# Kernel tuning notes

Measured on AMD Instinct MI355X. Metric: run time of the kernel, lower is better.

Reference implementation:

```python
import jax, jax.numpy as jnp
import numpy as np

N_NODES = 50000
IN_C, HID, N_CLS = 128, 128, 16
N_EDGES = 800000


def gcn_conv(x, W, b, src, dst, deg_inv_sqrt, n_nodes):
    # PyG GCNConv: h = x @ W; out[dst] += norm * h[src]; out += b
    h = x @ W                                   # [N, out_c]
    norm = deg_inv_sqrt[src] * deg_inv_sqrt[dst]  # [E]
    msgs = h[src] * norm[:, None]               # gather + scale, [E, out_c]
    out = jax.ops.segment_sum(msgs, dst, num_segments=n_nodes)
    return out + b


def setup_inputs() -> dict:
    key = jax.random.key(0)
    k1, k2, k3, k4, k5 = jax.random.split(key, 5)
    x = jax.random.normal(k1, (N_NODES, IN_C), dtype=jnp.float32)
    edge_index = jax.random.randint(k2, (2, N_EDGES), 0, N_NODES, dtype=jnp.int64)
    # glorot-ish params (torch.manual_seed(1234) in source only affects init values)
    def lin(k, fan_in, fan_out):
        s = 1.0 / np.sqrt(fan_in)
        kw, kb = jax.random.split(k)
        W = jax.random.uniform(kw, (fan_in, fan_out), minval=-s, maxval=s, dtype=jnp.float32)
        b = jax.random.uniform(kb, (fan_out,), minval=-s, maxval=s, dtype=jnp.float32)
        return W, b
    W1, b1 = lin(k3, IN_C, HID)
    W2, b2 = lin(k4, HID, HID)
    Wh, bh = lin(k5, HID, N_CLS)
    return {"x": x, "edge_index": edge_index, "W1": W1, "b1": b1,
            "W2": W2, "b2": b2, "Wh": Wh, "bh": bh}


def reference(x, edge_index, W1, b1, W2, b2, Wh, bh):
    n = x.shape[0]
    # add self-loops (PyG GCNConv default add_self_loops=True)
    loops = jnp.arange(n, dtype=edge_index.dtype)
    src = jnp.concatenate([edge_index[0], loops])
    dst = jnp.concatenate([edge_index[1], loops])
    # symmetric normalization D^{-1/2} (A+I) D^{-1/2}; degree over dst with unit weights
    deg = jax.ops.segment_sum(jnp.ones(src.shape[0], dtype=x.dtype), dst, num_segments=n)
    dis = jnp.where(deg > 0, jax.lax.rsqrt(deg), 0.0)
    h = gcn_conv(x, W1, b1, src, dst, dis, n)
    h = jax.nn.relu(h)
    h = gcn_conv(h, W2, b2, src, dst, dis, n)
    h = jax.nn.relu(h)
    return h @ Wh + bh
```

## Files before the change

kernel.cpp:

```cpp
#include <hip/hip_runtime.h>

#define CH 128
#define NCLS 16
#define CHK 16
#define NCHUNK 8
#define ECAP 131072

typedef __attribute__((ext_vector_type(8))) short bf16x8;
typedef __attribute__((ext_vector_type(4))) float f32x4;

__device__ inline ushort f2bf(float f) {
    unsigned u = __float_as_uint(f);
    unsigned r = u + 0x7fffu + ((u >> 16) & 1u);
    return (ushort)(r >> 16);
}
__device__ inline float bf2f(ushort b) {
    return __uint_as_float(((unsigned)b) << 16);
}

__global__ __launch_bounds__(256) void prep_kernel(
    const float* __restrict__ W1, const float* __restrict__ W2,
    ushort* __restrict__ w1hi, ushort* __restrict__ w1lo,
    ushort* __restrict__ w2hi, ushort* __restrict__ w2lo,
    int* __restrict__ cnt, int* __restrict__ pcnt, int* __restrict__ galloc,
    float* __restrict__ bufA, int n, int nbz) {
    int b = blockIdx.x, tid = threadIdx.x;
    if (b < 128) {
        const float* W = (b < 64) ? W1 : W2;
        ushort* Whi = (b < 64) ? w1hi : w2hi;
        ushort* Wlo = (b < 64) ? w1lo : w2lo;
        int t = ((b & 63) << 8) + tid;
        int k = t >> 7, nn = t & 127;
        float v = W[t];
        ushort h = f2bf(v);
        Whi[nn * CH + k] = h;
        Wlo[nn * CH + k] = f2bf(v - bf2f(h));
    } else if (b < 128 + nbz) {
        int i = (b - 128) * 256 + tid;
        if (i < n) cnt[i] = 0;
    } else {
        if (tid < NCHUNK * CHK) {
            int c = tid >> 4, ch = tid & 15;
            bufA[((size_t)c * (n + 1) + n) * CHK + ch] = 0.0f;
        }
        if (tid < 8) pcnt[tid] = 0;
        if (tid == 8) *galloc = 0;
    }
}

__global__ __launch_bounds__(256) void bucketcount_kernel(
    const int* __restrict__ src, const int* __restrict__ dst,
    unsigned* __restrict__ ebuf, int* __restrict__ pcnt,
    int* __restrict__ cnt, int E, float p8n) {
    __shared__ int lpos[8];
    __shared__ int lbase[8];
    int tid = threadIdx.x;
    if (tid < 8) lpos[tid] = 0;
    __syncthreads();
    int i0 = (blockIdx.x * 256 + tid) * 4;
    int part[4]; int off[4]; unsigned pk[4]; int c = 0;
    if (i0 + 3 < E) {
        int4 s4 = *(const int4*)&src[i0];
        int4 d4 = *(const int4*)&dst[i0];
        int ss[4] = {s4.x, s4.y, s4.z, s4.w};
        int dd[4] = {d4.x, d4.y, d4.z, d4.w};
        c = 4;
#pragma unroll
        for (int k = 0; k < 4; k++) {
            part[k] = min(7, (int)((float)dd[k] * p8n));
            pk[k] = ((unsigned)dd[k] << 16) | (unsigned)ss[k];
            off[k] = atomicAdd(&lpos[part[k]], 1);
            atomicAdd(&cnt[dd[k]], 1);
        }
    } else {
        for (int k = 0; k < 4 && i0 + k < E; k++) {
            int s = src[i0 + k], d = dst[i0 + k];
            part[c] = min(7, (int)((float)d * p8n));
            pk[c] = ((unsigned)d << 16) | (unsigned)s;
            off[c] = atomicAdd(&lpos[part[c]], 1);
            atomicAdd(&cnt[d], 1);
            c++;
        }
    }
    __syncthreads();
    if (tid < 8) lbase[tid] = atomicAdd(&pcnt[tid], lpos[tid]);
    __syncthreads();
    for (int k = 0; k < c; k++) {
        int idx = lbase[part[k]] + off[k];
        if (idx < ECAP) ebuf[(size_t)part[k] * ECAP + idx] = pk[k];
    }
}

__global__ __launch_bounds__(256) void place_kernel(
    const int* __restrict__ cnt, int* __restrict__ rsp,
    int* __restrict__ cursor, int* __restrict__ galloc,
    ushort* __restrict__ esrc, int n) {
    __shared__ int lds[256];
    __shared__ int gbase;
    int t = threadIdx.x;
    int i = blockIdx.x * 256 + t;
    int c = (i < n) ? cnt[i] : 0;
    int sz = (i < n) ? ((c + 8) & ~7) : 0;
    lds[t] = sz;
    __syncthreads();
    for (int off = 1; off < 256; off <<= 1) {
        int x = (t >= off) ? lds[t - off] : 0;
        __syncthreads();
        lds[t] += x;
        __syncthreads();
    }
    int incl = lds[t];
    if (t == 255) gbase = atomicAdd(galloc, incl);
    __syncthreads();
    int base = gbase + incl - sz;
    if (i < n) {
        rsp[i] = base;
        cursor[i] = base + 1;
        esrc[base] = (ushort)i;
        for (int p = base + 1 + c; p < base + sz; p++) esrc[p] = (ushort)n;
    }
}

template <bool RELU_IN>
__device__ __forceinline__ void gemm_body(
    int bx, int by, const float* __restrict__ A,
    const ushort* __restrict__ Bthi, const ushort* __restrict__ Btlo,
    const int* __restrict__ cntp, float* __restrict__ C, int n_rows) {
    const int tid = threadIdx.x;
    const int bm0 = bx * 256;
    const int wv = tid >> 6;
    const int lane = tid & 63;
    const int col = lane & 15;
    const int quad = lane >> 4;
    const int rbase = bm0 + wv * 64 + col;
    const int ntBase = by * 4;

    f32x4 acc[4][4];
#pragma unroll
    for (int m = 0; m < 4; m++)
#pragma unroll
        for (int t = 0; t < 4; t++) acc[m][t] = (f32x4){0.f, 0.f, 0.f, 0.f};

#pragma unroll
    for (int k0 = 0; k0 < 4; k0++) {
        const int kb = k0 * 32 + quad * 8;
        bf16x8 ah[4], al[4];
#pragma unroll
        for (int m = 0; m < 4; m++) {
            int arow = rbase + m * 16;
            bool av = (arow < n_rows);
            const float* __restrict__ Ap = A + (size_t)arow * CH + kb;
            float4 f0 = av ? *(const float4*)Ap       : make_float4(0.f, 0.f, 0.f, 0.f);
            float4 f1 = av ? *(const float4*)(Ap + 4) : make_float4(0.f, 0.f, 0.f, 0.f);
            if (RELU_IN) {
                f0.x = fmaxf(f0.x, 0.f); f0.y = fmaxf(f0.y, 0.f);
                f0.z = fmaxf(f0.z, 0.f); f0.w = fmaxf(f0.w, 0.f);
                f1.x = fmaxf(f1.x, 0.f); f1.y = fmaxf(f1.y, 0.f);
                f1.z = fmaxf(f1.z, 0.f); f1.w = fmaxf(f1.w, 0.f);
            }
            float fa[8] = {f0.x, f0.y, f0.z, f0.w, f1.x, f1.y, f1.z, f1.w};
#pragma unroll
            for (int j = 0; j < 8; j++) {
                ushort h = f2bf(fa[j]);
                ah[m][j] = (short)h;
                al[m][j] = (short)f2bf(fa[j] - bf2f(h));
            }
        }
#pragma unroll
        for (int t = 0; t < 4; t++) {
            const int boff = ((ntBase + t) * 16 + col) * CH + kb;
            bf16x8 bh = *(const bf16x8*)&Bthi[boff];
            bf16x8 bl = *(const bf16x8*)&Btlo[boff];
#pragma unroll
            for (int m = 0; m < 4; m++) {
                acc[m][t] = __builtin_amdgcn_mfma_f32_16x16x32_bf16(ah[m], bh, acc[m][t], 0, 0, 0);
                acc[m][t] = __builtin_amdgcn_mfma_f32_16x16x32_bf16(ah[m], bl, acc[m][t], 0, 0, 0);
                acc[m][t] = __builtin_amdgcn_mfma_f32_16x16x32_bf16(al[m], bh, acc[m][t], 0, 0, 0);
            }
        }
    }

#pragma unroll
    for (int m = 0; m < 4; m++) {
#pragma unroll
        for (int reg = 0; reg < 4; reg++) {
            int gr = bm0 + wv * 64 + m * 16 + quad * 4 + reg;
            if (gr < n_rows) {
                float d = rsqrtf((float)cntp[gr] + 1.0f);
#pragma unroll
                for (int t = 0; t < 4; t++) {
                    int nt = ntBase + t;
                    C[((size_t)nt * (n_rows + 1) + gr) * CHK + col] = acc[m][t][reg] * d;
                }
            }
        }
    }
}

template <bool RELU_IN>
__global__ __launch_bounds__(256, 2) void gemmfill_kernel(
    const float* __restrict__ A, const ushort* __restrict__ Bthi,
    const ushort* __restrict__ Btlo, const int* __restrict__ cntp,
    float* __restrict__ C, int n_rows, int nbx, int gemmBlocks,
    const unsigned* __restrict__ ebuf, const int* __restrict__ pcnt,
    int* __restrict__ cursor, ushort* __restrict__ esrc) {
    int b = blockIdx.x;
    if (b < gemmBlocks) {
        gemm_body<RELU_IN>(b % nbx, b / nbx, A, Bthi, Btlo, cntp, C, n_rows);
    } else {
        int fb = b - gemmBlocks;
        int part = fb & 7;
        int m = min(pcnt[part], ECAP);
        const unsigned* bk = ebuf + (size_t)part * ECAP;
        for (int e = (fb >> 3) * 256 + (int)threadIdx.x; e < m; e += 256 * 256) {
            unsigned pe = bk[e];
            int p = atomicAdd(&cursor[pe >> 16], 1);
            esrc[p] = (ushort)(pe & 0xffffu);
        }
    }
}

__global__ __launch_bounds__(256) void gather_kernel(
    const int* __restrict__ rsp, const int* __restrict__ cnt,
    const ushort* __restrict__ esrc, const float* __restrict__ hC,
    const float* __restrict__ bias, float* __restrict__ out, int n) {
    int c = blockIdx.x & 7;
    int wv = threadIdx.x >> 6;
    int lane = threadIdx.x & 63;
    int g = lane >> 2;
    int q = lane & 3;
    int i = (blockIdx.x >> 3) * 64 + wv * 16 + g;
    bool valid = (i < n);
    int iw = valid ? i : 0;
    const float4* __restrict__ h4 = (const float4*)(hC + (size_t)c * (n + 1) * CHK);

    float warm = 0.f;
    {
        int nblk = (n + 63) >> 6;
        size_t p = (size_t)(blockIdx.x >> 3) * 256 + threadIdx.x;
        size_t sliceF4 = ((size_t)(n + 1) * CHK) >> 2;
        for (; p < sliceF4; p += (size_t)nblk * 256) {
            float4 v = h4[p];
            warm += v.x + v.y + v.z + v.w;
        }
    }

    int beg = valid ? rsp[iw] : 0;
    int cv  = valid ? cnt[iw] : -8;
    int pc  = (cv + 8) & ~7;
    float4 acc = make_float4(0.f, 0.f, 0.f, 0.f);
    for (int j = beg; j < beg + pc; j += 8) {
        ushort4 e0 = *(const ushort4*)&esrc[j];
        ushort4 e1 = *(const ushort4*)&esrc[j + 4];
        float4 v0 = h4[(size_t)e0.x * 4 + q];
        float4 v1 = h4[(size_t)e0.y * 4 + q];
        float4 v2 = h4[(size_t)e0.z * 4 + q];
        float4 v3 = h4[(size_t)e0.w * 4 + q];
        float4 v4 = h4[(size_t)e1.x * 4 + q];
        float4 v5 = h4[(size_t)e1.y * 4 + q];
        float4 v6 = h4[(size_t)e1.z * 4 + q];
        float4 v7 = h4[(size_t)e1.w * 4 + q];
        acc.x += v0.x; acc.y += v0.y; acc.z += v0.z; acc.w += v0.w;
        acc.x += v1.x; acc.y += v1.y; acc.z += v1.z; acc.w += v1.w;
        acc.x += v2.x; acc.y += v2.y; acc.z += v2.z; acc.w += v2.w;
        acc.x += v3.x; acc.y += v3.y; acc.z += v3.z; acc.w += v3.w;
        acc.x += v4.x; acc.y += v4.y; acc.z += v4.z; acc.w += v4.w;
        acc.x += v5.x; acc.y += v5.y; acc.z += v5.z; acc.w += v5.w;
        acc.x += v6.x; acc.y += v6.y; acc.z += v6.z; acc.w += v6.w;
        acc.x += v7.x; acc.y += v7.y; acc.z += v7.z; acc.w += v7.w;
    }
    __asm__ volatile("" : : "v"(warm));
    if (valid) {
        float di = rsqrtf((float)cv + 1.0f);
        float4 bv = ((const float4*)bias)[c * 4 + q];
        f32x4 o;
        o[0] = bv.x + di * acc.x;
        o[1] = bv.y + di * acc.y;
        o[2] = bv.z + di * acc.z;
        o[3] = bv.w + di * acc.w;
        __builtin_nontemporal_store(o, (f32x4*)&((float4*)out)[(size_t)iw * 32 + c * 4 + q]);
    }
}

__global__ __launch_bounds__(256) void head_kernel(
    const float* __restrict__ A, const float* __restrict__ Wh,
    const float* __restrict__ bh, float* __restrict__ out, int n) {
    __shared__ float Ws[CH * NCLS];
    __shared__ float As[16][129];
    const int tid = threadIdx.x;
    const int n0 = blockIdx.x * 16;
#pragma unroll
    for (int i = 0; i < 8; i++) {
        int l = tid + i * 256;
        Ws[l] = Wh[l];
    }
#pragma unroll
    for (int i = 0; i < 8; i++) {
        int l = tid + i * 256;
        int r = l >> 7, c = l & 127;
        int gr = n0 + r;
        As[r][c] = (gr < n) ? fmaxf(A[(size_t)gr * CH + c], 0.0f) : 0.0f;
    }
    __syncthreads();
    int r = tid >> 4, c = tid & 15;
    float acc = bh[c];
#pragma unroll
    for (int k = 0; k < CH; k++) acc = fmaf(As[r][k], Ws[k * NCLS + c], acc);
    int gr = n0 + r;
    if (gr < n) out[(size_t)gr * NCLS + c] = acc;
}

extern "C" void kernel_launch(void* const* d_in, const int* in_sizes, int n_in,
                              void* d_out, int out_size, void* d_ws, size_t ws_size,
                              hipStream_t stream) {
    const float* x  = (const float*)d_in[0];
    const int*   ei = (const int*)d_in[1];
    const float* W1 = (const float*)d_in[2];
    const float* b1 = (const float*)d_in[3];
    const float* W2 = (const float*)d_in[4];
    const float* b2 = (const float*)d_in[5];
    const float* Wh = (const float*)d_in[6];
    const float* bh = (const float*)d_in[7];
    float* out = (float*)d_out;

    const int n = in_sizes[0] / CH;
    const int E = in_sizes[1] / 2;
    const int* src = ei;
    const int* dst = ei + E;

    ushort* w1hi = (ushort*)d_ws;
    ushort* w1lo = w1hi + CH * CH;
    ushort* w2hi = w1lo + CH * CH;
    ushort* w2lo = w2hi + CH * CH;
    float* bufA = (float*)(w2lo + CH * CH);
    float* bufB = bufA + (size_t)(n + 1) * CH;
    int* cnt    = (int*)(bufB + (size_t)n * CH);
    int* rsp    = cnt + n;
    int* cursor = rsp + n;
    int* pcnt   = cursor + n;
    int* galloc = pcnt + 8;
    ushort* esrc = (ushort*)(pcnt + 16);
    unsigned* ebuf = (unsigned*)bufB;

    const int B = 256;
    const int nbz = (n + B - 1) / B;
    const int nbx = (n + 255) / 256;
    const int gemmBlocks = nbx * 2;
    const float p8n = 8.0f / (float)n;

    prep_kernel<<<128 + nbz + 1, B, 0, stream>>>(W1, W2, w1hi, w1lo, w2hi, w2lo,
                                                 cnt, pcnt, galloc, bufA, n, nbz);
    bucketcount_kernel<<<(E + 1023) / 1024, B, 0, stream>>>(src, dst, ebuf, pcnt,
                                                            cnt, E, p8n);
    place_kernel<<<nbz, B, 0, stream>>>(cnt, rsp, cursor, galloc, esrc, n);

    const int gatherGrid = NCHUNK * ((n + 63) / 64);

    gemmfill_kernel<false><<<gemmBlocks + 2048, B, 0, stream>>>(
        x, w1hi, w1lo, cnt, bufA, n, nbx, gemmBlocks, ebuf, pcnt, cursor, esrc);
    gather_kernel<<<gatherGrid, B, 0, stream>>>(rsp, cnt, esrc, bufA, b1, bufB, n);
    gemmfill_kernel<true><<<gemmBlocks, B, 0, stream>>>(
        bufB, w2hi, w2lo, cnt, bufA, n, nbx, gemmBlocks, ebuf, pcnt, cursor, esrc);
    gather_kernel<<<gatherGrid, B, 0, stream>>>(rsp, cnt, esrc, bufA, b2, bufB, n);
    head_kernel<<<(n + 15) / 16, B, 0, stream>>>(bufB, Wh, bh, out, n);
}
```

Measured before the change: 296.2 us.

## Split degree counting and CSR fill out of bucket and GEMM kernels

The bucketing kernel no longer does global atomic degree counts. A separate count kernel now reads the partitioned edge buffer, where dst-localized partitions may give better atomic locality. The CSR fill that ran inside the first GEMM launch is moved to its own kernel. The GEMM becomes a standalone kernel with 128-row tiles, a 2D grid and launch bounds of 4 blocks per CU for higher occupancy. The cost is two extra launches and an extra pass over the edge buffer, and the fill no longer overlaps with the first GEMM.

```diff
diff --git a/kernel.cpp b/kernel.cpp
--- a/kernel.cpp
+++ b/kernel.cpp
@@ -48,10 +48,9 @@
     }
 }
 
-__global__ __launch_bounds__(256) void bucketcount_kernel(
+__global__ __launch_bounds__(256) void bucket_kernel(
     const int* __restrict__ src, const int* __restrict__ dst,
-    unsigned* __restrict__ ebuf, int* __restrict__ pcnt,
-    int* __restrict__ cnt, int E, float p8n) {
+    unsigned* __restrict__ ebuf, int* __restrict__ pcnt, int E, float p8n) {
     __shared__ int lpos[8];
     __shared__ int lbase[8];
     int tid = threadIdx.x;
@@ -70,7 +69,6 @@
             part[k] = min(7, (int)((float)dd[k] * p8n));
             pk[k] = ((unsigned)dd[k] << 16) | (unsigned)ss[k];
             off[k] = atomicAdd(&lpos[part[k]], 1);
-            atomicAdd(&cnt[dd[k]], 1);
         }
     } else {
         for (int k = 0; k < 4 && i0 + k < E; k++) {
@@ -78,7 +76,6 @@
             part[c] = min(7, (int)((float)d * p8n));
             pk[c] = ((unsigned)d << 16) | (unsigned)s;
             off[c] = atomicAdd(&lpos[part[c]], 1);
-            atomicAdd(&cnt[d], 1);
             c++;
         }
     }
@@ -88,6 +85,18 @@
     for (int k = 0; k < c; k++) {
         int idx = lbase[part[k]] + off[k];
         if (idx < ECAP) ebuf[(size_t)part[k] * ECAP + idx] = pk[k];
+    }
+}
+
+__global__ __launch_bounds__(256) void count_kernel(
+    const unsigned* __restrict__ ebuf, const int* __restrict__ pcnt,
+    int* __restrict__ cnt) {
+    int part = blockIdx.x & 7;
+    int m = min(pcnt[part], ECAP);
+    const unsigned* bk = ebuf + (size_t)part * ECAP;
+    int stride = (int)(gridDim.x >> 3) * 256;
+    for (int e = (int)(blockIdx.x >> 3) * 256 + threadIdx.x; e < m; e += stride) {
+        atomicAdd(&cnt[bk[e] >> 16], 1);
     }
 }
 
@@ -121,32 +130,46 @@
     }
 }
 
+__global__ __launch_bounds__(256) void fill_kernel(
+    const unsigned* __restrict__ ebuf, const int* __restrict__ pcnt,
+    int* __restrict__ cursor, ushort* __restrict__ esrc) {
+    int part = blockIdx.x & 7;
+    int m = min(pcnt[part], ECAP);
+    const unsigned* bk = ebuf + (size_t)part * ECAP;
+    int stride = (int)(gridDim.x >> 3) * 256;
+    for (int e = (int)(blockIdx.x >> 3) * 256 + threadIdx.x; e < m; e += stride) {
+        unsigned pe = bk[e];
+        int p = atomicAdd(&cursor[pe >> 16], 1);
+        esrc[p] = (ushort)(pe & 0xffffu);
+    }
+}
+
 template <bool RELU_IN>
-__device__ __forceinline__ void gemm_body(
-    int bx, int by, const float* __restrict__ A,
-    const ushort* __restrict__ Bthi, const ushort* __restrict__ Btlo,
-    const int* __restrict__ cntp, float* __restrict__ C, int n_rows) {
+__global__ __launch_bounds__(256, 4) void gemm_mfma(
+    const float* __restrict__ A, const ushort* __restrict__ Bthi,
+    const ushort* __restrict__ Btlo, const int* __restrict__ cntp,
+    float* __restrict__ C, int n_rows) {
     const int tid = threadIdx.x;
-    const int bm0 = bx * 256;
+    const int bm0 = blockIdx.x * 128;
     const int wv = tid >> 6;
     const int lane = tid & 63;
     const int col = lane & 15;
     const int quad = lane >> 4;
-    const int rbase = bm0 + wv * 64 + col;
-    const int ntBase = by * 4;
-
-    f32x4 acc[4][4];
-#pragma unroll
-    for (int m = 0; m < 4; m++)
+    const int rbase = bm0 + wv * 32 + col;
+    const int ntBase = blockIdx.y * 4;
+
+    f32x4 acc[2][4];
+#pragma unroll
+    for (int m = 0; m < 2; m++)
 #pragma unroll
         for (int t = 0; t < 4; t++) acc[m][t] = (f32x4){0.f, 0.f, 0.f, 0.f};
 
 #pragma unroll
     for (int k0 = 0; k0 < 4; k0++) {
         const int kb = k0 * 32 + quad * 8;
-        bf16x8 ah[4], al[4];
-#pragma unroll
-        for (int m = 0; m < 4; m++) {
+        bf16x8 ah[2], al[2];
+#pragma unroll
+        for (int m = 0; m < 2; m++) {
             int arow = rbase + m * 16;
             bool av = (arow < n_rows);
             const float* __restrict__ Ap = A + (size_t)arow * CH + kb;
@@ -172,7 +195,7 @@
             bf16x8 bh = *(const bf16x8*)&Bthi[boff];
             bf16x8 bl = *(const bf16x8*)&Btlo[boff];
 #pragma unroll
-            for (int m = 0; m < 4; m++) {
+            for (int m = 0; m < 2; m++) {
                 acc[m][t] = __builtin_amdgcn_mfma_f32_16x16x32_bf16(ah[m], bh, acc[m][t], 0, 0, 0);
                 acc[m][t] = __builtin_amdgcn_mfma_f32_16x16x32_bf16(ah[m], bl, acc[m][t], 0, 0, 0);
                 acc[m][t] = __builtin_amdgcn_mfma_f32_16x16x32_bf16(al[m], bh, acc[m][t], 0, 0, 0);
@@ -181,10 +204,10 @@
     }
 
 #pragma unroll
-    for (int m = 0; m < 4; m++) {
+    for (int m = 0; m < 2; m++) {
 #pragma unroll
         for (int reg = 0; reg < 4; reg++) {
-            int gr = bm0 + wv * 64 + m * 16 + quad * 4 + reg;
+            int gr = bm0 + wv * 32 + m * 16 + quad * 4 + reg;
             if (gr < n_rows) {
                 float d = rsqrtf((float)cntp[gr] + 1.0f);
 #pragma unroll
@@ -193,29 +216,6 @@
                     C[((size_t)nt * (n_rows + 1) + gr) * CHK + col] = acc[m][t][reg] * d;
                 }
             }
-        }
-    }
-}
-
-template <bool RELU_IN>
-__global__ __launch_bounds__(256, 2) void gemmfill_kernel(
-    const float* __restrict__ A, const ushort* __restrict__ Bthi,
-    const ushort* __restrict__ Btlo, const int* __restrict__ cntp,
-    float* __restrict__ C, int n_rows, int nbx, int gemmBlocks,
-    const unsigned* __restrict__ ebuf, const int* __restrict__ pcnt,
-    int* __restrict__ cursor, ushort* __restrict__ esrc) {
-    int b = blockIdx.x;
-    if (b < gemmBlocks) {
-        gemm_body<RELU_IN>(b % nbx, b / nbx, A, Bthi, Btlo, cntp, C, n_rows);
-    } else {
-        int fb = b - gemmBlocks;
-        int part = fb & 7;
-        int m = min(pcnt[part], ECAP);
-        const unsigned* bk = ebuf + (size_t)part * ECAP;
-        for (int e = (fb >> 3) * 256 + (int)threadIdx.x; e < m; e += 256 * 256) {
-            unsigned pe = bk[e];
-            int p = atomicAdd(&cursor[pe >> 16], 1);
-            esrc[p] = (ushort)(pe & 0xffffu);
         }
     }
 }
@@ -344,23 +344,21 @@
 
     const int B = 256;
     const int nbz = (n + B - 1) / B;
-    const int nbx = (n + 255) / 256;
-    const int gemmBlocks = nbx * 2;
     const float p8n = 8.0f / (float)n;
 
     prep_kernel<<<128 + nbz + 1, B, 0, stream>>>(W1, W2, w1hi, w1lo, w2hi, w2lo,
                                                  cnt, pcnt, galloc, bufA, n, nbz);
-    bucketcount_kernel<<<(E + 1023) / 1024, B, 0, stream>>>(src, dst, ebuf, pcnt,
-                                                            cnt, E, p8n);
+    bucket_kernel<<<(E + 1023) / 1024, B, 0, stream>>>(src, dst, ebuf, pcnt, E, p8n);
+    count_kernel<<<2048, B, 0, stream>>>(ebuf, pcnt, cnt);
     place_kernel<<<nbz, B, 0, stream>>>(cnt, rsp, cursor, galloc, esrc, n);
-
+    fill_kernel<<<2048, B, 0, stream>>>(ebuf, pcnt, cursor, esrc);
+
+    const dim3 gemmGrid((n + 127) / 128, 2);
     const int gatherGrid = NCHUNK * ((n + 63) / 64);
 
-    gemmfill_kernel<false><<<gemmBlocks + 2048, B, 0, stream>>>(
-        x, w1hi, w1lo, cnt, bufA, n, nbx, gemmBlocks, ebuf, pcnt, cursor, esrc);
+    gemm_mfma<false><<<gemmGrid, B, 0, stream>>>(x, w1hi, w1lo, cnt, bufA, n);
     gather_kernel<<<gatherGrid, B, 0, stream>>>(rsp, cnt, esrc, bufA, b1, bufB, n);
-    gemmfill_kernel<true><<<gemmBlocks, B, 0, stream>>>(
-        bufB, w2hi, w2lo, cnt, bufA, n, nbx, gemmBlocks, ebuf, pcnt, cursor, esrc);
+    gemm_mfma<true><<<gemmGrid, B, 0, stream>>>(bufB, w2hi, w2lo, cnt, bufA, n);
     gather_kernel<<<gatherGrid, B, 0, stream>>>(rsp, cnt, esrc, bufA, b2, bufB, n);
     head_kernel<<<(n + 15) / 16, B, 0, stream>>>(bufB, Wh, bh, out, n);
 }
```

Measured after the change: 321.6 us. 8.6% more time.
